# Kernel tuning notes

Hardware: AMD Instinct MI355X
Metric: run time of the kernel (lower is better)

The kernel has to match this reference:

```python
import jax, jax.numpy as jnp
import numpy as np

B, L, V = 4, 1024, 1280
N_EMBD, N_BIN, N_HID = 768, 8, 32
HORIZON = 10.0


def setup_inputs() -> dict:
    key = jax.random.key(0)
    k_h, k_age, k_gap, k_tgt, k_w1, k_w2 = jax.random.split(key, 6)
    h = jax.random.normal(k_h, (B, L, N_EMBD), dtype=jnp.float32)
    # ages increase along a trajectory; gaps in [0, 2) years
    age = jnp.sort(jax.random.uniform(k_age, (B, L), dtype=jnp.float32) * 80.0, axis=-1)
    targets_age = age + jax.random.uniform(k_gap, (B, L), dtype=jnp.float32) * 2.0
    delta_t = targets_age - age  # passed to forward but unused (as in torch source)
    targets = jax.random.randint(k_tgt, (B, L), 0, V, dtype=jnp.int32)
    W1 = jax.random.normal(k_w1, (N_EMBD, N_BIN * N_HID), dtype=jnp.float32) * 0.02
    W2 = jax.random.normal(k_w2, (N_HID, V), dtype=jnp.float32) * 0.02
    return {"h": h, "age": age, "targets_age": targets_age, "delta_t": delta_t,
            "targets": targets, "W1": W1, "W2": W2}


def _time_to_event(age, targets_age, targets):
    # delta_full[b,i,j] = targets_age[b,j] - age[b,i]
    delta_full = targets_age[:, None, :] - age[:, :, None]  # (B,L,L)
    i_idx = jnp.arange(L)
    # torch.triu(diagonal=0): keep targets[b,j] where j>=i, else 0
    upper = (i_idx[None, :] >= i_idx[:, None])  # (L,L) mask, col>=row
    targets_exp = jnp.where(upper[None, :, :], targets[:, None, :], 0)  # (B,L,L)
    # scatter-reduce amin of position index j into vocab slot targets_exp[b,i,j]
    # sentinel L plays the role of torch's -1 (min over srcs ignores it; src<=L-1)
    b_ix = jnp.arange(B)[:, None, None]
    r_ix = i_idx[None, :, None]
    src = jnp.broadcast_to(i_idx[None, None, :], (B, L, L)).astype(jnp.int32)
    token_index = jnp.full((B, L, V), L, dtype=jnp.int32)
    token_index = token_index.at[b_ix, r_ix, targets_exp].min(src)
    no_event = token_index == L
    token_index = jnp.where(no_event, L - 1, token_index)  # (B,L,V)
    tte = jnp.take_along_axis(delta_full, token_index, axis=-1)  # (B,L,V)
    return tte, no_event, token_index


def reference(h, age, targets_age, delta_t, targets, W1, W2):
    # two dense projections: (B,L,E) -> (B,L,n_bin,n_hid) -> (B,L,n_bin,V)
    x = jnp.einsum('ble,eo->blo', h, W1).reshape(B, L, N_BIN, N_HID)
    logits = jnp.einsum('blnh,hv->blnv', x, W2)
    tte, no_event, _ = _time_to_event(age, targets_age, targets)
    edges = jnp.linspace(0.0, HORIZON, N_BIN + 1)
    lo = edges[:-1][None, None, :, None]
    hi = edges[1:][None, None, :, None]
    t = tte[:, :, None, :]  # (B,L,1,V)
    censor_mask = ((t >= lo) & (t < hi)) | no_event[:, :, None, :]  # (B,L,n_bin,V)
    return logits, tte, censor_mask
```

## Files before the change

kernel.cpp:

```cpp
#include <hip/hip_runtime.h>
#include <hip/hip_bf16.h>

#define B_   4
#define L_   1024
#define V_   1280
#define NE_  768
#define NB_  8
#define NH_  32
#define NO_  (NB_*NH_)
#define BL_  (B_*L_)

__global__ __launch_bounds__(256) void k1_gemm(const float* __restrict__ H,
                                               const float* __restrict__ W1,
                                               float* __restrict__ X) {
    __shared__ float As[16][64];
    __shared__ float Bs[16][64];

    const int t  = threadIdx.x;
    const int m0 = blockIdx.x * 64;
    const int n0 = blockIdx.y * 64;
    const int tx = t & 15;
    const int ty = t >> 4;

    const int lr = t >> 2;
    const int lq = t & 3;
    const int br = t >> 4;
    const int bq = t & 15;

    float acc[4][4];
#pragma unroll
    for (int r = 0; r < 4; ++r)
#pragma unroll
        for (int c = 0; c < 4; ++c) acc[r][c] = 0.0f;

    for (int k0 = 0; k0 < NE_; k0 += 16) {
        float4 av = *(const float4*)(H  + (size_t)(m0 + lr) * NE_ + k0 + lq * 4);
        float4 bv = *(const float4*)(W1 + (size_t)(k0 + br) * NO_ + n0 + bq * 4);
        __syncthreads();
        As[lq*4+0][lr] = av.x;
        As[lq*4+1][lr] = av.y;
        As[lq*4+2][lr] = av.z;
        As[lq*4+3][lr] = av.w;
        *(float4*)&Bs[br][bq*4] = bv;
        __syncthreads();
#pragma unroll
        for (int kk = 0; kk < 16; ++kk) {
            float4 a = *(float4*)&As[kk][ty*4];
            float4 b = *(float4*)&Bs[kk][tx*4];
            acc[0][0] += a.x*b.x; acc[0][1] += a.x*b.y; acc[0][2] += a.x*b.z; acc[0][3] += a.x*b.w;
            acc[1][0] += a.y*b.x; acc[1][1] += a.y*b.y; acc[1][2] += a.y*b.z; acc[1][3] += a.y*b.w;
            acc[2][0] += a.z*b.x; acc[2][1] += a.z*b.y; acc[2][2] += a.z*b.z; acc[2][3] += a.z*b.w;
            acc[3][0] += a.w*b.x; acc[3][1] += a.w*b.y; acc[3][2] += a.w*b.z; acc[3][3] += a.w*b.w;
        }
    }
#pragma unroll
    for (int r = 0; r < 4; ++r) {
        float4 v = make_float4(acc[r][0], acc[r][1], acc[r][2], acc[r][3]);
        *(float4*)&X[(size_t)(m0 + ty*4 + r) * NO_ + n0 + tx*4] = v;
    }
}

__global__ __launch_bounds__(256) void k2_logits(const float* __restrict__ X,
                                                 const float* __restrict__ W2,
                                                 float* __restrict__ outL) {
    __shared__ float xs[4 * NO_];
    __shared__ float w2s[NH_][256];

    const int t   = threadIdx.x;
    const int bl0 = blockIdx.x * 4;
    const int v0  = blockIdx.y * 256;

#pragma unroll
    for (int j = 0; j < 4; ++j)
        xs[j * 256 + t] = X[(size_t)bl0 * NO_ + j * 256 + t];
#pragma unroll
    for (int hh = 0; hh < NH_; ++hh)
        w2s[hh][t] = W2[(size_t)hh * V_ + v0 + t];
    __syncthreads();

    const int c4 = (t & 63) * 4;
    const int g  = t >> 6;

    float4 acc[NB_];
#pragma unroll
    for (int n = 0; n < NB_; ++n) acc[n] = make_float4(0.f, 0.f, 0.f, 0.f);

#pragma unroll
    for (int hh = 0; hh < NH_; ++hh) {
        float4 w = *(float4*)&w2s[hh][c4];
#pragma unroll
        for (int n = 0; n < NB_; ++n) {
            float xv = xs[g * 256 + n * 32 + hh];
            acc[n].x += xv * w.x;
            acc[n].y += xv * w.y;
            acc[n].z += xv * w.z;
            acc[n].w += xv * w.w;
        }
    }

    const size_t bl = (size_t)(bl0 + g);
#pragma unroll
    for (int n = 0; n < NB_; ++n)
        *(float4*)&outL[(bl * NB_ + n) * V_ + v0 + c4] = acc[n];
}

#define K3_S 32

__global__ __launch_bounds__(256) void k3_tte(const float* __restrict__ age,
                                              const float* __restrict__ tage,
                                              const int*   __restrict__ targets,
                                              float* __restrict__ outT,
                                              float* __restrict__ outM) {
    __shared__ int   tg[L_];
    __shared__ float ta[L_];
    __shared__ float ag[K3_S];

    const int t      = threadIdx.x;
    const int v      = blockIdx.x * 256 + t;
    const int istart = blockIdx.y * K3_S;
    const int iend   = istart + K3_S;
    const int b      = blockIdx.z;

    for (int j = t; j < L_; j += 256) {
        tg[j] = targets[(size_t)b * L_ + j];
        ta[j] = tage[(size_t)b * L_ + j];
    }
    if (t < K3_S) ag[t] = age[(size_t)b * L_ + istart + t];
    __syncthreads();

    int cur = L_;
    for (int i = L_ - 1; i >= istart; --i) {
        const int ti = tg[i];
        if (ti == v) cur = i;
        if (i < iend) {
            int idx = cur;
            if (v == 0 && i >= 1) idx = 0;
            const bool noev = (idx == L_);
            const int  ic   = noev ? (L_ - 1) : idx;
            const float tte = ta[ic] - ag[i - istart];

            outT[((size_t)(b * L_ + i)) * V_ + v] = tte;

            const size_t mb = ((size_t)(b * L_ + i)) * NB_ * V_ + v;
#pragma unroll
            for (int n = 0; n < NB_; ++n) {
                const float lo = n * 1.25f;
                const float hi = (n + 1) * 1.25f;
                const bool in_bin = (tte >= lo) && (tte < hi);
                outM[mb + (size_t)n * V_] = (in_bin || noev) ? 1.0f : 0.0f;
            }
        }
    }
}

extern "C" void kernel_launch(void* const* d_in, const int* in_sizes, int n_in,
                              void* d_out, int out_size, void* d_ws, size_t ws_size,
                              hipStream_t stream) {
    const float* h       = (const float*)d_in[0];
    const float* age     = (const float*)d_in[1];
    const float* tage    = (const float*)d_in[2];
    const int*   targets = (const int*)  d_in[4];
    const float* W1      = (const float*)d_in[5];
    const float* W2      = (const float*)d_in[6];

    float* out  = (float*)d_out;
    float* outL = out;
    float* outT = out + (size_t)BL_ * NB_ * V_;
    float* outM = outT + (size_t)BL_ * V_;

    float* X = (float*)d_ws;

    k1_gemm  <<<dim3(BL_/64, NO_/64), 256, 0, stream>>>(h, W1, X);
    k2_logits<<<dim3(BL_/4, V_/256),  256, 0, stream>>>(X, W2, outL);
    k3_tte   <<<dim3(V_/256, L_/K3_S, B_), 256, 0, stream>>>(age, tage, targets, outT, outM);
}
```

Before: 476.7 us.

## Convert GEMMs to bf16 MFMA with a packing pre-pass

```diff
diff --git a/kernel.cpp b/kernel.cpp
--- a/kernel.cpp
+++ b/kernel.cpp
@@ -9,99 +9,123 @@
 #define NH_  32
 #define NO_  (NB_*NH_)
 #define BL_  (B_*L_)
-
-__global__ __launch_bounds__(256) void k1_gemm(const float* __restrict__ H,
+#define M2_  (BL_*NB_)
+
+typedef __attribute__((ext_vector_type(8))) short bf16x8;
+typedef __attribute__((ext_vector_type(4))) float floatx4;
+
+__device__ __forceinline__ unsigned short f2bf(float f) {
+    unsigned int u = __float_as_uint(f);
+    u += 0x7FFFu + ((u >> 16) & 1u);
+    return (unsigned short)(u >> 16);
+}
+
+#define H4_N   (BL_*NE_/4)
+#define W1T_N  (NO_*NE_)
+#define W2T_N  (V_*NH_)
+#define K0_TOT (H4_N + W1T_N + W2T_N)
+
+__global__ __launch_bounds__(256) void k0_pack(const float* __restrict__ h,
                                                const float* __restrict__ W1,
-                                               float* __restrict__ X) {
-    __shared__ float As[16][64];
-    __shared__ float Bs[16][64];
-
-    const int t  = threadIdx.x;
-    const int m0 = blockIdx.x * 64;
-    const int n0 = blockIdx.y * 64;
-    const int tx = t & 15;
-    const int ty = t >> 4;
-
-    const int lr = t >> 2;
-    const int lq = t & 3;
-    const int br = t >> 4;
-    const int bq = t & 15;
-
-    float acc[4][4];
-#pragma unroll
-    for (int r = 0; r < 4; ++r)
-#pragma unroll
-        for (int c = 0; c < 4; ++c) acc[r][c] = 0.0f;
-
-    for (int k0 = 0; k0 < NE_; k0 += 16) {
-        float4 av = *(const float4*)(H  + (size_t)(m0 + lr) * NE_ + k0 + lq * 4);
-        float4 bv = *(const float4*)(W1 + (size_t)(k0 + br) * NO_ + n0 + bq * 4);
+                                               const float* __restrict__ W2,
+                                               unsigned short* __restrict__ hb,
+                                               unsigned short* __restrict__ W1T,
+                                               unsigned short* __restrict__ W2T) {
+    int id = blockIdx.x * 256 + threadIdx.x;
+    if (id < H4_N) {
+        float4 v = ((const float4*)h)[id];
+        ushort4 o;
+        o.x = f2bf(v.x); o.y = f2bf(v.y); o.z = f2bf(v.z); o.w = f2bf(v.w);
+        ((ushort4*)hb)[id] = o;
+    } else if (id < H4_N + W1T_N) {
+        int j = id - H4_N;
+        int o = j / NE_;
+        int k = j - o * NE_;
+        W1T[j] = f2bf(W1[(size_t)k * NO_ + o]);
+    } else if (id < K0_TOT) {
+        int j = id - H4_N - W1T_N;
+        int v = j >> 5;
+        int k = j & 31;
+        W2T[j] = f2bf(W2[(size_t)k * V_ + v]);
+    }
+}
+
+__global__ __launch_bounds__(256) void k1_gemm(const unsigned short* __restrict__ hb,
+                                               const unsigned short* __restrict__ W1T,
+                                               unsigned short* __restrict__ Xb) {
+    __shared__ short A_lds[64][40];
+    __shared__ short Bt_lds[64][40];
+
+    const int t      = threadIdx.x;
+    const int m0     = blockIdx.x * 64;
+    const int n0     = blockIdx.y * 64;
+    const int l      = t & 63;
+    const int w      = t >> 6;
+    const int lane15 = l & 15;
+    const int quad   = l >> 4;
+
+    const int srow = t >> 2;
+    const int sq   = (t & 3) * 8;
+
+    const unsigned short* aptr = hb  + (size_t)(m0 + srow) * NE_ + sq;
+    const unsigned short* bptr = W1T + (size_t)(n0 + srow) * NE_ + sq;
+
+    floatx4 acc[4];
+#pragma unroll
+    for (int i = 0; i < 4; ++i) acc[i] = (floatx4){0.f, 0.f, 0.f, 0.f};
+
+    bf16x8 av = *(const bf16x8*)aptr;
+    bf16x8 bv = *(const bf16x8*)bptr;
+
+    for (int k0 = 0; k0 < NE_; k0 += 32) {
         __syncthreads();
-        As[lq*4+0][lr] = av.x;
-        As[lq*4+1][lr] = av.y;
-        As[lq*4+2][lr] = av.z;
-        As[lq*4+3][lr] = av.w;
-        *(float4*)&Bs[br][bq*4] = bv;
+        *(bf16x8*)&A_lds[srow][sq]  = av;
+        *(bf16x8*)&Bt_lds[srow][sq] = bv;
         __syncthreads();
-#pragma unroll
-        for (int kk = 0; kk < 16; ++kk) {
-            float4 a = *(float4*)&As[kk][ty*4];
-            float4 b = *(float4*)&Bs[kk][tx*4];
-            acc[0][0] += a.x*b.x; acc[0][1] += a.x*b.y; acc[0][2] += a.x*b.z; acc[0][3] += a.x*b.w;
-            acc[1][0] += a.y*b.x; acc[1][1] += a.y*b.y; acc[1][2] += a.y*b.z; acc[1][3] += a.y*b.w;
-            acc[2][0] += a.z*b.x; acc[2][1] += a.z*b.y; acc[2][2] += a.z*b.z; acc[2][3] += a.z*b.w;
-            acc[3][0] += a.w*b.x; acc[3][1] += a.w*b.y; acc[3][2] += a.w*b.z; acc[3][3] += a.w*b.w;
+        if (k0 + 32 < NE_) {
+            av = *(const bf16x8*)(aptr + k0 + 32);
+            bv = *(const bf16x8*)(bptr + k0 + 32);
         }
-    }
-#pragma unroll
-    for (int r = 0; r < 4; ++r) {
-        float4 v = make_float4(acc[r][0], acc[r][1], acc[r][2], acc[r][3]);
-        *(float4*)&X[(size_t)(m0 + ty*4 + r) * NO_ + n0 + tx*4] = v;
-    }
-}
-
-__global__ __launch_bounds__(256) void k2_logits(const float* __restrict__ X,
-                                                 const float* __restrict__ W2,
+        bf16x8 af = *(bf16x8*)&A_lds[w * 16 + lane15][quad * 8];
+#pragma unroll
+        for (int nt = 0; nt < 4; ++nt) {
+            bf16x8 bf = *(bf16x8*)&Bt_lds[nt * 16 + lane15][quad * 8];
+            acc[nt] = __builtin_amdgcn_mfma_f32_16x16x32_bf16(af, bf, acc[nt], 0, 0, 0);
+        }
+    }
+
+    const int rbase = m0 + w * 16 + quad * 4;
+#pragma unroll
+    for (int nt = 0; nt < 4; ++nt)
+#pragma unroll
+        for (int r = 0; r < 4; ++r)
+            Xb[(size_t)(rbase + r) * NO_ + n0 + nt * 16 + lane15] = f2bf(acc[nt][r]);
+}
+
+__global__ __launch_bounds__(256) void k2_logits(const unsigned short* __restrict__ Xb,
+                                                 const unsigned short* __restrict__ W2T,
                                                  float* __restrict__ outL) {
-    __shared__ float xs[4 * NO_];
-    __shared__ float w2s[NH_][256];
-
-    const int t   = threadIdx.x;
-    const int bl0 = blockIdx.x * 4;
-    const int v0  = blockIdx.y * 256;
-
-#pragma unroll
-    for (int j = 0; j < 4; ++j)
-        xs[j * 256 + t] = X[(size_t)bl0 * NO_ + j * 256 + t];
-#pragma unroll
-    for (int hh = 0; hh < NH_; ++hh)
-        w2s[hh][t] = W2[(size_t)hh * V_ + v0 + t];
-    __syncthreads();
-
-    const int c4 = (t & 63) * 4;
-    const int g  = t >> 6;
-
-    float4 acc[NB_];
-#pragma unroll
-    for (int n = 0; n < NB_; ++n) acc[n] = make_float4(0.f, 0.f, 0.f, 0.f);
-
-#pragma unroll
-    for (int hh = 0; hh < NH_; ++hh) {
-        float4 w = *(float4*)&w2s[hh][c4];
-#pragma unroll
-        for (int n = 0; n < NB_; ++n) {
-            float xv = xs[g * 256 + n * 32 + hh];
-            acc[n].x += xv * w.x;
-            acc[n].y += xv * w.y;
-            acc[n].z += xv * w.z;
-            acc[n].w += xv * w.w;
-        }
-    }
-
-    const size_t bl = (size_t)(bl0 + g);
-#pragma unroll
-    for (int n = 0; n < NB_; ++n)
-        *(float4*)&outL[(bl * NB_ + n) * V_ + v0 + c4] = acc[n];
+    const int t      = threadIdx.x;
+    const int m0     = blockIdx.x * 64;
+    const int l      = t & 63;
+    const int w      = t >> 6;
+    const int lane15 = l & 15;
+    const int quad   = l >> 4;
+
+    const int m = m0 + w * 16 + lane15;
+    const bf16x8 af = *(const bf16x8*)(Xb + (size_t)m * NH_ + quad * 8);
+
+    const int rbase = m0 + w * 16 + quad * 4;
+
+#pragma unroll 4
+    for (int nt = 0; nt < V_ / 16; ++nt) {
+        bf16x8 bf = *(const bf16x8*)(W2T + (size_t)(nt * 16 + lane15) * NH_ + quad * 8);
+        floatx4 c = (floatx4){0.f, 0.f, 0.f, 0.f};
+        c = __builtin_amdgcn_mfma_f32_16x16x32_bf16(af, bf, c, 0, 0, 0);
+#pragma unroll
+        for (int r = 0; r < 4; ++r)
+            outL[(size_t)(rbase + r) * V_ + nt * 16 + lane15] = c[r];
+    }
 }
 
 #define K3_S 32
@@ -168,9 +192,14 @@
     float* outT = out + (size_t)BL_ * NB_ * V_;
     float* outM = outT + (size_t)BL_ * V_;
 
-    float* X = (float*)d_ws;
-
-    k1_gemm  <<<dim3(BL_/64, NO_/64), 256, 0, stream>>>(h, W1, X);
-    k2_logits<<<dim3(BL_/4, V_/256),  256, 0, stream>>>(X, W2, outL);
+    char* ws = (char*)d_ws;
+    unsigned short* hb  = (unsigned short*)(ws);
+    unsigned short* W1T = (unsigned short*)(ws + 6291456);
+    unsigned short* W2T = (unsigned short*)(ws + 6291456 + 393216);
+    unsigned short* Xb  = (unsigned short*)(ws + 6291456 + 393216 + 81920);
+
+    k0_pack  <<<(K0_TOT + 255) / 256, 256, 0, stream>>>(h, W1, W2, hb, W1T, W2T);
+    k1_gemm  <<<dim3(BL_/64, NO_/64), 256, 0, stream>>>(hb, W1T, Xb);
+    k2_logits<<<M2_/64, 256, 0, stream>>>(Xb, W2T, outL);
     k3_tte   <<<dim3(V_/256, L_/K3_S, B_), 256, 0, stream>>>(age, tage, targets, outT, outM);
 }
```

Result: faster. 423.1 us (-11.3%).
